# Kernel tuning notes

Hardware: AMD Instinct MI355X
Metric: run time of the kernel (lower is better)

## Reference

```python
import jax, jax.numpy as jnp
import numpy as np

NUM_TOKENS = 8192
DIM = 256
BETA = 0.25
DECAY = 0.99
EPS = 1e-05


def setup_inputs() -> dict:
    key = jax.random.key(0)
    k1, k2 = jax.random.split(key, 2)
    z = jax.random.normal(k1, (16, DIM, 32, 32), dtype=jnp.float32)
    embedding = jax.random.normal(k2, (NUM_TOKENS, DIM), dtype=jnp.float32)
    cluster_size = jnp.zeros((NUM_TOKENS,), dtype=jnp.float32)
    ema_w = embedding  # module init copies embed_init into both embedding and ema_w
    return {"z": z, "embedding": embedding, "cluster_size": cluster_size, "ema_w": ema_w}


def reference(z, embedding, cluster_size, ema_w):
    # z: [B, D, H, W] -> [B, H, W, D]
    zp = jnp.transpose(z, (0, 2, 3, 1))
    zf = zp.reshape(-1, DIM)  # [N, D]
    # squared euclidean distances [N, K] via ||z||^2 + ||e||^2 - 2 z.e
    d = (jnp.sum(zf * zf, axis=1, keepdims=True)
         + jnp.sum(embedding * embedding, axis=1)
         - 2.0 * (zf @ embedding.T))
    idx = jnp.argmin(d, axis=1)  # [N]
    z_q = embedding[idx].reshape(zp.shape)  # [B, H, W, D]

    # training-mode EMA statistics (pure-functional: returned as new states)
    counts = jax.ops.segment_sum(jnp.ones(zf.shape[0], dtype=zf.dtype), idx,
                                 num_segments=NUM_TOKENS)
    embed_sum = jax.ops.segment_sum(zf, idx, num_segments=NUM_TOKENS)  # [K, D]
    cs = cluster_size * DECAY + (1.0 - DECAY) * counts
    new_ema_w = ema_w * DECAY + (1.0 - DECAY) * embed_sum
    # torch evaluates sum AFTER add_(eps): denom = sum(cs + eps) + K*eps
    cs = cs + EPS
    new_cluster_size = cs / (jnp.sum(cs) + NUM_TOKENS * EPS)
    new_embedding = new_ema_w / new_cluster_size[:, None]

    loss = BETA * jnp.mean((jax.lax.stop_gradient(z_q) - zp) ** 2)
    # straight-through estimator
    z_q_st = zp + jax.lax.stop_gradient(z_q - zp)
    out = jnp.transpose(z_q_st, (0, 3, 1, 2))  # back to [B, D, H, W]
    return out, loss, idx, new_cluster_size, new_ema_w, new_embedding
```

## Files before the change

kernel.cpp:

```cpp
#include <hip/hip_runtime.h>

#define N_TOK   16384
#define K_CODES 8192
#define DIMS    256

#define OUT_OFF  0
#define LOSS_OFF 4194304
#define IDX_OFF  4194305
#define NCS_OFF  4210689
#define NEMA_OFF 4218881
#define NEMB_OFF 6316033

#define WS_ZFRAG  0u
#define WS_EFRAG  16777216u
#define WS_ENORM  25165824u
#define WS_PVAL   25198592u
#define WS_PIDX   25460736u
#define WS_IDXI   25722880u
#define WS_CNT    25788416u
#define WS_CS     25821184u
#define WS_OFFS   25853952u
#define WS_WPOS   25886720u
#define WS_TLIST  25919488u
#define WS_DENOM  25985024u

typedef _Float16 f16x8 __attribute__((ext_vector_type(8)));
typedef float    f32x16 __attribute__((ext_vector_type(16)));

union HU { _Float16 h; unsigned short u; };

static __device__ inline void split_f32(float x, unsigned short& hi, unsigned short& lo) {
    HU a; a.h = (_Float16)x;
    float r = (x - (float)a.h) * 2048.0f;
    HU b; b.h = (_Float16)r;
    hi = a.u; lo = b.u;
}

static __device__ inline float join_f16(unsigned short h, unsigned short l) {
    HU a, b; a.u = h; b.u = l;
    return (float)a.h + (float)b.h * 4.8828125e-4f;
}

#define GLD16(gp, lp) __builtin_amdgcn_global_load_lds( \
    (const __attribute__((address_space(1))) unsigned int*)(gp), \
    (__attribute__((address_space(3))) unsigned int*)(lp), 16, 0, 0)

__global__ __launch_bounds__(256) void cvt_z_kernel(const float* __restrict__ z,
                                                    unsigned short* __restrict__ zfrag,
                                                    float* __restrict__ loss_cell,
                                                    double* __restrict__ denom) {
    __shared__ float T[64][65];
    const int t = threadIdx.x;
    const int hg = blockIdx.x & 15, dg = (blockIdx.x >> 4) & 3, b = blockIdx.x >> 6;
    if (blockIdx.x == 0 && t == 0) { *loss_cell = 0.f; *denom = 0.0; }
    const int c4 = (t & 15) * 4, r0 = t >> 4;
    const float* zb = z + (((size_t)(b * 256 + dg * 64)) << 10) + hg * 64;
#pragma unroll
    for (int p = 0; p < 4; ++p) {
        const int r = r0 + p * 16;
        const float4 v = *(const float4*)(zb + ((size_t)r << 10) + c4);
        T[r][c4] = v.x; T[r][c4 + 1] = v.y; T[r][c4 + 2] = v.z; T[r][c4 + 3] = v.w;
    }
    __syncthreads();
    const int tr = t & 63, dc = (t >> 6) * 16;
    const int tile = b * 16 + hg;
    const int tg = tile * 2 + (tr >> 5), l31 = tr & 31;
    const int ks = dg * 4 + (dc >> 4);
    unsigned short hb[16], lb[16];
#pragma unroll
    for (int j = 0; j < 16; ++j) split_f32(T[dc + j][tr], hb[j], lb[j]);
#pragma unroll
    for (int lv = 0; lv < 2; ++lv) {
        const unsigned short* src = lv ? lb : hb;
        unsigned short* dst = zfrag + (size_t)((tg * 2 + lv) * 16 + ks) * 512;
        *(uint4*)(dst + l31 * 8)       = ((const uint4*)src)[0];
        *(uint4*)(dst + 256 + l31 * 8) = ((const uint4*)src)[1];
    }
}

__global__ __launch_bounds__(256) void cvt_e_enorm(const float* __restrict__ emb,
                                                   unsigned short* __restrict__ efrag,
                                                   float* __restrict__ enorm,
                                                   int* __restrict__ cnt) {
    __shared__ double red[256];
    const int t = threadIdx.x, g = blockIdx.x;
    const int lane = t & 63, q = t >> 6;
    const int l31 = lane & 31, lhi = lane >> 5;
    if (g < 32) cnt[g * 256 + t] = 0;
    const float* rowp = emb + (size_t)(g * 32 + l31) * 256 + lhi * 8;
    double s = 0.0;
#pragma unroll
    for (int kk = 0; kk < 4; ++kk) {
        const int ks = q * 4 + kk;
        const float4 a = *(const float4*)(rowp + ks * 16);
        const float4 bq = *(const float4*)(rowp + ks * 16 + 4);
        const float vv[8] = {a.x, a.y, a.z, a.w, bq.x, bq.y, bq.z, bq.w};
        unsigned short hb[8], lb[8];
#pragma unroll
        for (int j = 0; j < 8; ++j) {
            split_f32(vv[j], hb[j], lb[j]);
            s += (double)vv[j] * (double)vv[j];
        }
        *(uint4*)(efrag + (size_t)((g * 2 + 0) * 16 + ks) * 512 + lane * 8) = *(const uint4*)hb;
        *(uint4*)(efrag + (size_t)((g * 2 + 1) * 16 + ks) * 512 + lane * 8) = *(const uint4*)lb;
    }
    red[t] = s;
    __syncthreads();
    if (t < 32) {
        double acc = 0.0;
#pragma unroll
        for (int qq = 0; qq < 4; ++qq) acc += red[qq * 64 + t] + red[qq * 64 + 32 + t];
        enorm[g * 32 + t] = (float)acc;
    }
}

__global__ __launch_bounds__(256, 2) void argmin_mfma(
    const unsigned short* __restrict__ zfrag, const unsigned short* __restrict__ efrag,
    const float* __restrict__ enorm, float* __restrict__ pval, int* __restrict__ pidx) {
    __shared__ __align__(16) unsigned short E[2][8192];
    __shared__ float en_s[2][64];

    const int tid = threadIdx.x, lane = tid & 63, wave = tid >> 6;
    const int tile = blockIdx.x & 127, csplit = blockIdx.x >> 7;
    const int token0 = tile * 128, code0 = csplit * 2048;

    f16x8 Zr[2][16];
    {
        const unsigned short* zb = zfrag + (size_t)(tile * 4 + wave) * 16384 + lane * 8;
#pragma unroll
        for (int lv = 0; lv < 2; ++lv)
#pragma unroll
            for (int ks = 0; ks < 16; ++ks)
                Zr[lv][ks] = *(const f16x8*)(zb + (lv * 16 + ks) * 512);
    }

    const int slv = wave >> 1, scg = wave & 1;

    float bv = 3.4e38f; int bi = 0;

#pragma unroll
    for (int ksl = 0; ksl < 4; ++ksl) {
        const unsigned short* sp = efrag +
            (size_t)(((csplit * 64 + scg) * 2 + slv) * 16 + ksl) * 512 + lane * 8;
        GLD16(sp, &E[0][(wave * 4 + ksl) * 512]);
    }
    if (tid < 64) en_s[0][tid] = enorm[code0 + tid];
    __syncthreads();

    for (int ct = 0; ct < 32; ++ct) {
        f32x16 acc_h[2], acc_l[2];
#pragma unroll
        for (int cg = 0; cg < 2; ++cg)
#pragma unroll
            for (int qq = 0; qq < 16; ++qq) { acc_h[cg][qq] = 0.f; acc_l[cg][qq] = 0.f; }

#pragma unroll
        for (int kc = 0; kc < 4; ++kc) {
            const int p = (ct * 4 + kc) & 1;
            if (!(ct == 31 && kc == 3)) {
                const int nch = ct * 4 + kc + 1;
                const int nct = nch >> 2, nkc = nch & 3;
                const int g = csplit * 64 + nct * 2 + scg;
#pragma unroll
                for (int ksl = 0; ksl < 4; ++ksl) {
                    const unsigned short* sp = efrag +
                        (size_t)((g * 2 + slv) * 16 + nkc * 4 + ksl) * 512 + lane * 8;
                    GLD16(sp, &E[p ^ 1][(wave * 4 + ksl) * 512]);
                }
            }
            if (kc == 0 && ct < 31 && tid < 64)
                en_s[(ct + 1) & 1][tid] = enorm[code0 + (ct + 1) * 64 + tid];

#pragma unroll
            for (int ksl = 0; ksl < 4; ++ksl) {
                const int ks = kc * 4 + ksl;
                f16x8 ae[2][2];
#pragma unroll
                for (int lv = 0; lv < 2; ++lv)
#pragma unroll
                    for (int cg = 0; cg < 2; ++cg)
                        ae[lv][cg] = *(const f16x8*)&E[p][((lv * 2 + cg) * 4 + ksl) * 512 + lane * 8];
#pragma unroll
                for (int cg = 0; cg < 2; ++cg) {
                    acc_h[cg] = __builtin_amdgcn_mfma_f32_32x32x16_f16(ae[0][cg], Zr[0][ks], acc_h[cg], 0, 0, 0);
                    acc_l[cg] = __builtin_amdgcn_mfma_f32_32x32x16_f16(ae[0][cg], Zr[1][ks], acc_l[cg], 0, 0, 0);
                    acc_l[cg] = __builtin_amdgcn_mfma_f32_32x32x16_f16(ae[1][cg], Zr[0][ks], acc_l[cg], 0, 0, 0);
                }
            }
            if (kc == 3) {
                const int rbase = 4 * (lane >> 5);
#pragma unroll
                for (int cg = 0; cg < 2; ++cg)
#pragma unroll
                    for (int r = 0; r < 16; ++r) {
                        const int cl = cg * 32 + (r & 3) + 8 * (r >> 2) + rbase;
                        const float s = en_s[ct & 1][cl] -
                            2.0f * (acc_h[cg][r] + acc_l[cg][r] * 4.8828125e-4f);
                        const int code = code0 + ct * 64 + cl;
                        if (s < bv) { bv = s; bi = code; }
                    }
            }
            __syncthreads();
        }
    }
    {
        const float ov = __shfl_xor(bv, 32);
        const int   oi = __shfl_xor(bi, 32);
        if (ov < bv || (ov == bv && oi < bi)) { bv = ov; bi = oi; }
    }
    if (lane < 32) {
        const int n = token0 + wave * 32 + lane;
        pval[csplit * N_TOK + n] = bv;
        pidx[csplit * N_TOK + n] = bi;
    }
}

__global__ __launch_bounds__(256) void combine4_kernel(
    const float* __restrict__ pval, const int* __restrict__ pidx,
    int* __restrict__ idx_i, float* __restrict__ idx_f, int* __restrict__ cnt) {
    const int n = blockIdx.x * 256 + threadIdx.x;
    float bv = pval[n]; int bi = pidx[n];
#pragma unroll
    for (int s = 1; s < 4; ++s) {
        const float v = pval[s * N_TOK + n];
        const int i = pidx[s * N_TOK + n];
        if (v < bv || (v == bv && i < bi)) { bv = v; bi = i; }
    }
    idx_i[n] = bi;
    idx_f[n] = (float)bi;
    atomicAdd(&cnt[bi], 1);
}

__global__ __launch_bounds__(256) void scan_kernel(const int* __restrict__ cnt,
                                                   int* __restrict__ offs,
                                                   int* __restrict__ wpos) {
    __shared__ int part[256];
    const int tid = threadIdx.x;
    const int base = tid * 32;
    int loc[32];
    int s = 0;
#pragma unroll
    for (int j = 0; j < 32; ++j) { loc[j] = cnt[base + j]; s += loc[j]; }
    part[tid] = s;
    __syncthreads();
    for (int off = 1; off < 256; off <<= 1) {
        int v = 0;
        if (tid >= off) v = part[tid - off];
        __syncthreads();
        if (tid >= off) part[tid] += v;
        __syncthreads();
    }
    int run = (tid > 0) ? part[tid - 1] : 0;
#pragma unroll
    for (int j = 0; j < 32; ++j) {
        offs[base + j] = run;
        wpos[base + j] = run;
        run += loc[j];
    }
}

__global__ __launch_bounds__(256) void scatter_cs(
    const int* __restrict__ idx_i, int* __restrict__ wpos, int* __restrict__ tlist,
    const float* __restrict__ cluster_size, const int* __restrict__ cnt,
    float* __restrict__ cs, double* __restrict__ denom) {
    __shared__ double red[256];
    const int t = threadIdx.x, b = blockIdx.x;
    if (b < 64) {
        const int n = b * 256 + t;
        const int k = idx_i[n];
        tlist[atomicAdd(&wpos[k], 1)] = n;
    } else {
        const int k = (b - 64) * 256 + t;
        const float v = cluster_size[k] * 0.99f + 0.01f * (float)cnt[k] + 1e-5f;
        cs[k] = v;
        red[t] = (double)v;
        __syncthreads();
        for (int s2 = 128; s2; s2 >>= 1) {
            if (t < s2) red[t] += red[t + s2];
            __syncthreads();
        }
        if (t == 0) atomicAdd(denom, red[0]);
    }
}

__global__ __launch_bounds__(256) void nema_gather(
    const unsigned short* __restrict__ zfrag,
    const int* __restrict__ offs, const int* __restrict__ cnt, const int* __restrict__ tlist,
    const float* __restrict__ ema_w, const float* __restrict__ cs,
    const double* __restrict__ denom, float* __restrict__ ncs_out,
    float* __restrict__ nema_out, float* __restrict__ nemb_out,
    const float* __restrict__ z, const float* __restrict__ emb,
    const int* __restrict__ idx_i, float* __restrict__ out, float* __restrict__ loss_cell) {
    __shared__ float redf[256];
    const int t = threadIdx.x;
    if (blockIdx.x < 2048) {
        const int lane = t & 63, wave = t >> 6;
        const int k = blockIdx.x * 4 + wave;
        const int l31 = lane & 31, sel = lane >> 5;
        const int beg = offs[k], c = cnt[k];
        float acc[8] = {0.f, 0.f, 0.f, 0.f, 0.f, 0.f, 0.f, 0.f};
        for (int i = 0; i < c; ++i) {
            const int tok = tlist[beg + i];
            const int tg = tok >> 5, tl = tok & 31;
            const uint4 v = *(const uint4*)(zfrag +
                (size_t)((tg * 2 + sel) * 16 + (l31 >> 1)) * 512 + (l31 & 1) * 256 + tl * 8);
            uint4 o;
            o.x = __shfl_xor((int)v.x, 32); o.y = __shfl_xor((int)v.y, 32);
            o.z = __shfl_xor((int)v.z, 32); o.w = __shfl_xor((int)v.w, 32);
            if (lane < 32) {
                const unsigned short* hp = (const unsigned short*)&v;
                const unsigned short* lp = (const unsigned short*)&o;
#pragma unroll
                for (int j = 0; j < 8; ++j) acc[j] += join_f16(hp[j], lp[j]);
            }
        }
        const float dn = (float)(*denom) + (float)K_CODES * 1e-5f;
        const float ncs = cs[k] / dn;
        if (lane == 0) ncs_out[k] = ncs;
        if (lane < 32) {
            const size_t off = ((size_t)k << 8) + l31 * 8;
#pragma unroll
            for (int j = 0; j < 8; ++j) {
                const float ne = ema_w[off + j] * 0.99f + 0.01f * acc[j];
                nema_out[off + j] = ne;
                nemb_out[off + j] = ne / ncs;
            }
        }
    } else {
        const int gb = blockIdx.x - 2048;
        const int n0 = (gb >> 2) * 64;
        const int dg = (gb & 3) * 64;
        const int b = n0 >> 10, hw0 = n0 & 1023;
        const int lane = t & 63, w = t >> 6;
        const int n = n0 + lane;
        const int k = idx_i[n];
        const float* zb = z + ((size_t)b << 18) + hw0 + lane;
        float* ob = out + ((size_t)b << 18) + hw0 + lane;
        float ls = 0.f;
#pragma unroll 4
        for (int d = dg + w; d < dg + 64; d += 4) {
            const float zv = zb[(size_t)d << 10];
            const float ev = emb[((size_t)k << 8) + d];
            ob[(size_t)d << 10] = ev;
            const float df = ev - zv;
            ls += df * df;
        }
        redf[t] = ls;
        __syncthreads();
        for (int s2 = 128; s2; s2 >>= 1) {
            if (t < s2) redf[t] += redf[t + s2];
            __syncthreads();
        }
        if (t == 0) atomicAdd(loss_cell, redf[0] * (0.25f / 4194304.0f));
    }
}

extern "C" void kernel_launch(void* const* d_in, const int* in_sizes, int n_in,
                              void* d_out, int out_size, void* d_ws, size_t ws_size,
                              hipStream_t stream) {
    const float* z            = (const float*)d_in[0];
    const float* emb          = (const float*)d_in[1];
    const float* cluster_size = (const float*)d_in[2];
    const float* ema_w        = (const float*)d_in[3];
    float* out = (float*)d_out;
    char*  wsb = (char*)d_ws;

    unsigned short* zfrag = (unsigned short*)(wsb + WS_ZFRAG);
    unsigned short* efrag = (unsigned short*)(wsb + WS_EFRAG);
    float*  enorm  = (float*)(wsb + WS_ENORM);
    float*  pval   = (float*)(wsb + WS_PVAL);
    int*    pidx   = (int*)(wsb + WS_PIDX);
    int*    idx_i  = (int*)(wsb + WS_IDXI);
    int*    cnt    = (int*)(wsb + WS_CNT);
    float*  cs     = (float*)(wsb + WS_CS);
    int*    offs   = (int*)(wsb + WS_OFFS);
    int*    wpos   = (int*)(wsb + WS_WPOS);
    int*    tlist  = (int*)(wsb + WS_TLIST);
    double* denom  = (double*)(wsb + WS_DENOM);

    cvt_z_kernel<<<1024, 256, 0, stream>>>(z, zfrag, out + LOSS_OFF, denom);
    cvt_e_enorm<<<256, 256, 0, stream>>>(emb, efrag, enorm, cnt);
    argmin_mfma<<<512, 256, 0, stream>>>(zfrag, efrag, enorm, pval, pidx);
    combine4_kernel<<<N_TOK / 256, 256, 0, stream>>>(pval, pidx, idx_i,
                                                     out + IDX_OFF, cnt);
    scan_kernel<<<1, 256, 0, stream>>>(cnt, offs, wpos);
    scatter_cs<<<96, 256, 0, stream>>>(idx_i, wpos, tlist, cluster_size, cnt, cs, denom);
    nema_gather<<<3072, 256, 0, stream>>>(zfrag, offs, cnt, tlist, ema_w, cs, denom,
                                          out + NCS_OFF, out + NEMA_OFF, out + NEMB_OFF,
                                          z, emb, idx_i, out + OUT_OFF, out + LOSS_OFF);
}
```

Baseline: 418.8 us.

## Replace split-fp16 argmin with single-fp16 candidate filter plus exact rescore

The distance GEMM now runs one fp16 MFMA per tile instead of three hi/lo split products. It collects every code whose approximate distance falls within a fixed margin of the running best into per-token candidate lists. A new rescore kernel recomputes exact split-precision dot products for those candidates and picks the argmin, replacing the four-way partial combine. This cuts matrix-core work by about two thirds but adds atomics, candidate storage and a rescoring pass. Correctness depends on the margin covering the fp16 error and on candidate lists not overflowing their caps.

```diff
diff --git a/kernel.cpp b/kernel.cpp
--- a/kernel.cpp
+++ b/kernel.cpp
@@ -3,6 +3,7 @@
 #define N_TOK   16384
 #define K_CODES 8192
 #define DIMS    256
+#define MARGIN  0.25f
 
 #define OUT_OFF  0
 #define LOSS_OFF 4194304
@@ -14,15 +15,15 @@
 #define WS_ZFRAG  0u
 #define WS_EFRAG  16777216u
 #define WS_ENORM  25165824u
-#define WS_PVAL   25198592u
-#define WS_PIDX   25460736u
-#define WS_IDXI   25722880u
-#define WS_CNT    25788416u
-#define WS_CS     25821184u
-#define WS_OFFS   25853952u
-#define WS_WPOS   25886720u
-#define WS_TLIST  25919488u
-#define WS_DENOM  25985024u
+#define WS_CNT    25198592u
+#define WS_CS     25231360u
+#define WS_OFFS   25264128u
+#define WS_WPOS   25296896u
+#define WS_TLIST  25329664u
+#define WS_IDXI   25395200u
+#define WS_GCNT   25460736u
+#define WS_DENOM  25526272u
+#define WS_GCAND  25526784u
 
 typedef _Float16 f16x8 __attribute__((ext_vector_type(8)));
 typedef float    f32x16 __attribute__((ext_vector_type(16)));
@@ -81,12 +82,14 @@
 __global__ __launch_bounds__(256) void cvt_e_enorm(const float* __restrict__ emb,
                                                    unsigned short* __restrict__ efrag,
                                                    float* __restrict__ enorm,
-                                                   int* __restrict__ cnt) {
+                                                   int* __restrict__ cnt,
+                                                   int* __restrict__ gcnt) {
     __shared__ double red[256];
     const int t = threadIdx.x, g = blockIdx.x;
     const int lane = t & 63, q = t >> 6;
     const int l31 = lane & 31, lhi = lane >> 5;
     if (g < 32) cnt[g * 256 + t] = 0;
+    if (g < 64) gcnt[g * 256 + t] = 0;
     const float* rowp = emb + (size_t)(g * 32 + l31) * 256 + lhi * 8;
     double s = 0.0;
 #pragma unroll
@@ -114,45 +117,43 @@
     }
 }
 
-__global__ __launch_bounds__(256, 2) void argmin_mfma(
+__global__ __launch_bounds__(256, 2) void argmin_approx(
     const unsigned short* __restrict__ zfrag, const unsigned short* __restrict__ efrag,
-    const float* __restrict__ enorm, float* __restrict__ pval, int* __restrict__ pidx) {
-    __shared__ __align__(16) unsigned short E[2][8192];
+    const float* __restrict__ enorm, int* __restrict__ gcnt,
+    unsigned short* __restrict__ gcand) {
+    __shared__ __align__(16) unsigned short E[2][4096];
     __shared__ float en_s[2][64];
+    __shared__ unsigned short lcand[128][32];
+    __shared__ int lcnt[128];
 
     const int tid = threadIdx.x, lane = tid & 63, wave = tid >> 6;
-    const int tile = blockIdx.x & 127, csplit = blockIdx.x >> 7;
+    const int tile = blockIdx.x >> 2, csplit = blockIdx.x & 3;
     const int token0 = tile * 128, code0 = csplit * 2048;
 
-    f16x8 Zr[2][16];
+    if (tid < 128) lcnt[tid] = 0;
+
+    f16x8 Zr[16];
     {
         const unsigned short* zb = zfrag + (size_t)(tile * 4 + wave) * 16384 + lane * 8;
 #pragma unroll
-        for (int lv = 0; lv < 2; ++lv)
-#pragma unroll
-            for (int ks = 0; ks < 16; ++ks)
-                Zr[lv][ks] = *(const f16x8*)(zb + (lv * 16 + ks) * 512);
-    }
-
-    const int slv = wave >> 1, scg = wave & 1;
-
-    float bv = 3.4e38f; int bi = 0;
-
-#pragma unroll
-    for (int ksl = 0; ksl < 4; ++ksl) {
-        const unsigned short* sp = efrag +
-            (size_t)(((csplit * 64 + scg) * 2 + slv) * 16 + ksl) * 512 + lane * 8;
-        GLD16(sp, &E[0][(wave * 4 + ksl) * 512]);
-    }
+        for (int ks = 0; ks < 16; ++ks) Zr[ks] = *(const f16x8*)(zb + ks * 512);
+    }
+
+#pragma unroll
+    for (int cg = 0; cg < 2; ++cg)
+        GLD16(efrag + ((size_t)(csplit * 64 + cg) * 32 + wave) * 512 + lane * 8,
+              &E[0][(cg * 4 + wave) * 512]);
     if (tid < 64) en_s[0][tid] = enorm[code0 + tid];
     __syncthreads();
 
+    float bv = 3.4e38f;
+
     for (int ct = 0; ct < 32; ++ct) {
-        f32x16 acc_h[2], acc_l[2];
+        f32x16 acc[2];
 #pragma unroll
         for (int cg = 0; cg < 2; ++cg)
 #pragma unroll
-            for (int qq = 0; qq < 16; ++qq) { acc_h[cg][qq] = 0.f; acc_l[cg][qq] = 0.f; }
+            for (int qq = 0; qq < 16; ++qq) acc[cg][qq] = 0.f;
 
 #pragma unroll
         for (int kc = 0; kc < 4; ++kc) {
@@ -160,75 +161,107 @@
             if (!(ct == 31 && kc == 3)) {
                 const int nch = ct * 4 + kc + 1;
                 const int nct = nch >> 2, nkc = nch & 3;
-                const int g = csplit * 64 + nct * 2 + scg;
-#pragma unroll
-                for (int ksl = 0; ksl < 4; ++ksl) {
-                    const unsigned short* sp = efrag +
-                        (size_t)((g * 2 + slv) * 16 + nkc * 4 + ksl) * 512 + lane * 8;
-                    GLD16(sp, &E[p ^ 1][(wave * 4 + ksl) * 512]);
-                }
+#pragma unroll
+                for (int cg = 0; cg < 2; ++cg)
+                    GLD16(efrag + ((size_t)(csplit * 64 + nct * 2 + cg) * 32 + nkc * 4 + wave) * 512 + lane * 8,
+                          &E[p ^ 1][(cg * 4 + wave) * 512]);
             }
             if (kc == 0 && ct < 31 && tid < 64)
                 en_s[(ct + 1) & 1][tid] = enorm[code0 + (ct + 1) * 64 + tid];
 
 #pragma unroll
             for (int ksl = 0; ksl < 4; ++ksl) {
-                const int ks = kc * 4 + ksl;
-                f16x8 ae[2][2];
-#pragma unroll
-                for (int lv = 0; lv < 2; ++lv)
-#pragma unroll
-                    for (int cg = 0; cg < 2; ++cg)
-                        ae[lv][cg] = *(const f16x8*)&E[p][((lv * 2 + cg) * 4 + ksl) * 512 + lane * 8];
-#pragma unroll
-                for (int cg = 0; cg < 2; ++cg) {
-                    acc_h[cg] = __builtin_amdgcn_mfma_f32_32x32x16_f16(ae[0][cg], Zr[0][ks], acc_h[cg], 0, 0, 0);
-                    acc_l[cg] = __builtin_amdgcn_mfma_f32_32x32x16_f16(ae[0][cg], Zr[1][ks], acc_l[cg], 0, 0, 0);
-                    acc_l[cg] = __builtin_amdgcn_mfma_f32_32x32x16_f16(ae[1][cg], Zr[0][ks], acc_l[cg], 0, 0, 0);
-                }
+                const f16x8 ae0 = *(const f16x8*)&E[p][(0 * 4 + ksl) * 512 + lane * 8];
+                const f16x8 ae1 = *(const f16x8*)&E[p][(1 * 4 + ksl) * 512 + lane * 8];
+                acc[0] = __builtin_amdgcn_mfma_f32_32x32x16_f16(ae0, Zr[kc * 4 + ksl], acc[0], 0, 0, 0);
+                acc[1] = __builtin_amdgcn_mfma_f32_32x32x16_f16(ae1, Zr[kc * 4 + ksl], acc[1], 0, 0, 0);
             }
             if (kc == 3) {
                 const int rbase = 4 * (lane >> 5);
+                const float* ens = en_s[ct & 1];
 #pragma unroll
                 for (int cg = 0; cg < 2; ++cg)
 #pragma unroll
                     for (int r = 0; r < 16; ++r) {
                         const int cl = cg * 32 + (r & 3) + 8 * (r >> 2) + rbase;
-                        const float s = en_s[ct & 1][cl] -
-                            2.0f * (acc_h[cg][r] + acc_l[cg][r] * 4.8828125e-4f);
-                        const int code = code0 + ct * 64 + cl;
-                        if (s < bv) { bv = s; bi = code; }
+                        const float sv = ens[cl] - 2.0f * acc[cg][r];
+                        acc[cg][r] = sv;
+                        if (sv < bv) bv = sv;
                     }
+                const float ob = __shfl_xor(bv, 32);
+                const float thr = fminf(bv, ob) + MARGIN;
+                const int tl = wave * 32 + (lane & 31);
+#pragma unroll
+                for (int cg = 0; cg < 2; ++cg)
+#pragma unroll
+                    for (int r = 0; r < 16; ++r)
+                        if (acc[cg][r] < thr) {
+                            const int cl = cg * 32 + (r & 3) + 8 * (r >> 2) + rbase;
+                            const int code = code0 + ct * 64 + cl;
+                            const int pp = atomicAdd(&lcnt[tl], 1);
+                            if (pp < 32) lcand[tl][pp] = (unsigned short)code;
+                            else {
+                                const int gp = atomicAdd(&gcnt[token0 + tl], 1);
+                                if (gp < 64) gcand[(size_t)(token0 + tl) * 64 + gp] = (unsigned short)code;
+                            }
+                        }
             }
             __syncthreads();
         }
     }
+    if (lane < 32) {
+        const int tl = wave * 32 + lane;
+        const int token = token0 + tl;
+        const int L = min(lcnt[tl], 32);
+        const int base = atomicAdd(&gcnt[token], L);
+        for (int i = 0; i < L; ++i) {
+            const int gp = base + i;
+            if (gp < 64) gcand[(size_t)token * 64 + gp] = lcand[tl][i];
+        }
+    }
+}
+
+__global__ __launch_bounds__(256) void rescore_kernel(
+    const unsigned short* __restrict__ zfrag, const unsigned short* __restrict__ efrag,
+    const float* __restrict__ enorm, const int* __restrict__ gcnt,
+    const unsigned short* __restrict__ gcand, int* __restrict__ idx_i,
+    float* __restrict__ idx_f, int* __restrict__ cnt) {
+    const int lane = threadIdx.x & 63, wave = threadIdx.x >> 6;
+    const int t = blockIdx.x * 4 + wave;
+    const int ks = lane >> 2, khalf = (lane >> 1) & 1, j0 = (lane & 1) * 4;
+    const int loff = khalf * 256 + j0;
+    const int tg = t >> 5, tl = t & 31;
+    float zf[4];
     {
-        const float ov = __shfl_xor(bv, 32);
-        const int   oi = __shfl_xor(bi, 32);
-        if (ov < bv || (ov == bv && oi < bi)) { bv = ov; bi = oi; }
-    }
-    if (lane < 32) {
-        const int n = token0 + wave * 32 + lane;
-        pval[csplit * N_TOK + n] = bv;
-        pidx[csplit * N_TOK + n] = bi;
-    }
-}
-
-__global__ __launch_bounds__(256) void combine4_kernel(
-    const float* __restrict__ pval, const int* __restrict__ pidx,
-    int* __restrict__ idx_i, float* __restrict__ idx_f, int* __restrict__ cnt) {
-    const int n = blockIdx.x * 256 + threadIdx.x;
-    float bv = pval[n]; int bi = pidx[n];
-#pragma unroll
-    for (int s = 1; s < 4; ++s) {
-        const float v = pval[s * N_TOK + n];
-        const int i = pidx[s * N_TOK + n];
-        if (v < bv || (v == bv && i < bi)) { bv = v; bi = i; }
-    }
-    idx_i[n] = bi;
-    idx_f[n] = (float)bi;
-    atomicAdd(&cnt[bi], 1);
+        const ushort4 hv = *(const ushort4*)(zfrag + (size_t)((tg * 2 + 0) * 16 + ks) * 512 + loff + tl * 8);
+        const ushort4 lv = *(const ushort4*)(zfrag + (size_t)((tg * 2 + 1) * 16 + ks) * 512 + loff + tl * 8);
+        const unsigned short* hp = (const unsigned short*)&hv;
+        const unsigned short* lp = (const unsigned short*)&lv;
+#pragma unroll
+        for (int j = 0; j < 4; ++j) zf[j] = join_f16(hp[j], lp[j]);
+    }
+    const int C = min(gcnt[t], 64);
+    float best = 3.4e38f; int besti = 0;
+    for (int i = 0; i < C; ++i) {
+        const int c = gcand[(size_t)t * 64 + i];
+        const int g = c >> 5, cl = c & 31;
+        const ushort4 he = *(const ushort4*)(efrag + (size_t)((g * 2 + 0) * 16 + ks) * 512 + loff + cl * 8);
+        const ushort4 le = *(const ushort4*)(efrag + (size_t)((g * 2 + 1) * 16 + ks) * 512 + loff + cl * 8);
+        const unsigned short* hp = (const unsigned short*)&he;
+        const unsigned short* lp = (const unsigned short*)&le;
+        float dot = 0.f;
+#pragma unroll
+        for (int j = 0; j < 4; ++j) dot += zf[j] * join_f16(hp[j], lp[j]);
+#pragma unroll
+        for (int off = 32; off; off >>= 1) dot += __shfl_xor(dot, off);
+        const float s = enorm[c] - 2.0f * dot;
+        if (s < best || (s == best && c < besti)) { best = s; besti = c; }
+    }
+    if (lane == 0) {
+        idx_i[t] = besti;
+        idx_f[t] = (float)besti;
+        atomicAdd(&cnt[besti], 1);
+    }
 }
 
 __global__ __launch_bounds__(256) void scan_kernel(const int* __restrict__ cnt,
@@ -368,21 +401,21 @@
     unsigned short* zfrag = (unsigned short*)(wsb + WS_ZFRAG);
     unsigned short* efrag = (unsigned short*)(wsb + WS_EFRAG);
     float*  enorm  = (float*)(wsb + WS_ENORM);
-    float*  pval   = (float*)(wsb + WS_PVAL);
-    int*    pidx   = (int*)(wsb + WS_PIDX);
-    int*    idx_i  = (int*)(wsb + WS_IDXI);
     int*    cnt    = (int*)(wsb + WS_CNT);
     float*  cs     = (float*)(wsb + WS_CS);
     int*    offs   = (int*)(wsb + WS_OFFS);
     int*    wpos   = (int*)(wsb + WS_WPOS);
     int*    tlist  = (int*)(wsb + WS_TLIST);
+    int*    idx_i  = (int*)(wsb + WS_IDXI);
+    int*    gcnt   = (int*)(wsb + WS_GCNT);
     double* denom  = (double*)(wsb + WS_DENOM);
+    unsigned short* gcand = (unsigned short*)(wsb + WS_GCAND);
 
     cvt_z_kernel<<<1024, 256, 0, stream>>>(z, zfrag, out + LOSS_OFF, denom);
-    cvt_e_enorm<<<256, 256, 0, stream>>>(emb, efrag, enorm, cnt);
-    argmin_mfma<<<512, 256, 0, stream>>>(zfrag, efrag, enorm, pval, pidx);
-    combine4_kernel<<<N_TOK / 256, 256, 0, stream>>>(pval, pidx, idx_i,
-                                                     out + IDX_OFF, cnt);
+    cvt_e_enorm<<<256, 256, 0, stream>>>(emb, efrag, enorm, cnt, gcnt);
+    argmin_approx<<<512, 256, 0, stream>>>(zfrag, efrag, enorm, gcnt, gcand);
+    rescore_kernel<<<4096, 256, 0, stream>>>(zfrag, efrag, enorm, gcnt, gcand,
+                                             idx_i, out + IDX_OFF, cnt);
     scan_kernel<<<1, 256, 0, stream>>>(cnt, offs, wpos);
     scatter_cs<<<96, 256, 0, stream>>>(idx_i, wpos, tlist, cluster_size, cnt, cs, denom);
     nema_gather<<<3072, 256, 0, stream>>>(zfrag, offs, cnt, tlist, ema_w, cs, denom,
```

Result: slower. 433.5 us (+3.5%).
